# Kernel tuning notes

Measured on AMD Instinct MI355X. Metric: run time of the kernel, lower is better.

The kernel has to match this reference:

```python
import jax, jax.numpy as jnp
import numpy as np

BLANK = 4
NEG = -1.0e30  # log-space 'zero'


def _ctc_loss(log_probs, targets, input_lengths, target_lengths):
    # log_probs: (N, T, C) raw logits -> module applies log_softmax then transposes to (T, N, C)
    lp = jax.nn.log_softmax(log_probs, axis=-1)
    lp = jnp.transpose(lp, (1, 0, 2))  # (T, N, C)
    T, N, C = lp.shape
    S = targets.shape[1]
    L = 2 * S + 1  # extended label length (blanks interleaved)

    # extended label sequence: blank, y1, blank, y2, ..., yS, blank  -> (N, L)
    ext = jnp.full((N, L), BLANK, dtype=targets.dtype).at[:, 1::2].set(targets)

    # gather per-step log-probs of extended labels: (T, N, L)
    lp_ext = jnp.take_along_axis(lp, jnp.broadcast_to(ext[None], (T, N, L)), axis=2)

    # skip transition (k-2 -> k) allowed iff ext[k] != blank and ext[k] != ext[k-2]
    ext_m2 = jnp.pad(ext[:, :-2], ((0, 0), (2, 0)), constant_values=BLANK)
    skip = (ext != BLANK) & (ext != ext_m2)
    skip = skip.at[:, :2].set(False)

    # alpha at t=0: only positions 0 (blank) and 1 (first label) reachable
    alpha0 = jnp.full((N, L), NEG, dtype=lp.dtype)
    alpha0 = alpha0.at[:, 0].set(lp_ext[0, :, 0]).at[:, 1].set(lp_ext[0, :, 1])

    neg_col = jnp.full((N, 1), NEG, dtype=lp.dtype)

    def step(alpha, xs):
        t, lpe = xs  # lpe: (N, L)
        s1 = jnp.concatenate([neg_col, alpha[:, :-1]], axis=1)
        s2 = jnp.concatenate([neg_col, neg_col, alpha[:, :-2]], axis=1)
        a = jnp.logaddexp(alpha, s1)
        a = jnp.logaddexp(a, jnp.where(skip, s2, NEG))
        new = a + lpe
        # freeze alpha once past this sequence's input length
        alpha = jnp.where((t < input_lengths)[:, None], new, alpha)
        return alpha, None

    ts = jnp.arange(1, T)
    alpha, _ = jax.lax.scan(step, alpha0, (ts, lp_ext[1:]))

    idx = jnp.arange(N)
    last = 2 * target_lengths  # final blank position; last label is at 2L-1
    l_label = alpha[idx, last - 1]
    l_blank = alpha[idx, last]
    nll = -jnp.logaddexp(l_label, l_blank)  # per-sequence negative log-likelihood

    # reduction='mean': divide each loss by its target length, then mean over batch
    return jnp.mean(nll / target_lengths.astype(nll.dtype))


def setup_inputs() -> dict:
    key = jax.random.key(0)
    k1, k2, k3, k4 = jax.random.split(key, 4)
    N, T, C, S = 32, 1600, 1024, 200
    log_probs = jax.random.normal(k1, (N, T, C), dtype=jnp.float32)
    # targets in [0, C) excluding blank index 4
    t = jax.random.randint(k2, (N, S), 0, C - 1)
    targets = t + (t >= BLANK).astype(t.dtype)
    input_lengths = jax.random.randint(k3, (N,), 800, T + 1)
    target_lengths = jax.random.randint(k4, (N,), 50, S + 1)
    return {
        "log_probs": log_probs,
        "targets": targets,
        "input_lengths": input_lengths,
        "target_lengths": target_lengths,
    }


def reference(log_probs, targets, input_lengths, target_lengths):
    return _ctc_loss(log_probs, targets, input_lengths, target_lengths)
```

## Files before the change

kernel.cpp:

```cpp
#include <hip/hip_runtime.h>
#include <hip/hip_bf16.h>

#define N_    32
#define T_    1600
#define C_    1024
#define S_    200
#define L_    401
#define LP_   512
#define BLANK_ 4
#define LN2_  0.69314718055994531f
#define L2E_  1.44269504088896341f
#define DPF   8

#if __has_builtin(__builtin_amdgcn_exp2f)
#define EXP2(x) __builtin_amdgcn_exp2f(x)
#else
#define EXP2(x) exp2f(x)
#endif
#if __has_builtin(__builtin_amdgcn_rcpf)
#define RCP(x) __builtin_amdgcn_rcpf(x)
#else
#define RCP(x) (1.0f / (x))
#endif

__global__ __launch_bounds__(256)
void k_softmax_gather(const float* __restrict__ logits,
                      const int* __restrict__ targets,
                      const int* __restrict__ tgt_len,
                      float* __restrict__ P) {
  const int row  = blockIdx.x * 4 + (threadIdx.x >> 6);
  const int lane = threadIdx.x & 63;
  const int wv   = threadIdx.x >> 6;
  const int n    = row / T_;
  const float* x = logits + (size_t)row * C_;
  __shared__ float sh[4][C_];

  float4 v[4];
#pragma unroll
  for (int i = 0; i < 4; ++i)
    v[i] = reinterpret_cast<const float4*>(x)[i * 64 + lane];

  float mx = v[0].x;
#pragma unroll
  for (int i = 0; i < 4; ++i)
    mx = fmaxf(mx, fmaxf(fmaxf(v[i].x, v[i].y), fmaxf(v[i].z, v[i].w)));
#pragma unroll
  for (int i = 1; i < 64; i <<= 1) mx = fmaxf(mx, __shfl_xor(mx, i));

  float s = 0.0f;
#pragma unroll
  for (int i = 0; i < 4; ++i) {
    s += EXP2((v[i].x - mx) * L2E_) + EXP2((v[i].y - mx) * L2E_)
       + EXP2((v[i].z - mx) * L2E_) + EXP2((v[i].w - mx) * L2E_);
  }
#pragma unroll
  for (int i = 1; i < 64; i <<= 1) s += __shfl_xor(s, i);
  float rz = RCP(s);

#pragma unroll
  for (int i = 0; i < 4; ++i)
    reinterpret_cast<float4*>(sh[wv])[i * 64 + lane] = v[i];
  __syncthreads();

  const int* tg = targets + n * S_;
  const int lmax = 2 * tgt_len[n];
  float* out = P + (size_t)row * LP_;
#pragma unroll
  for (int i = 0; i < 8; ++i) {
    int l = lane + i * 64;
    float p = 0.0f;
    if (l <= lmax) {
      int c = (l & 1) ? tg[(l - 1) >> 1] : BLANK_;
      p = EXP2((sh[wv][c] - mx) * L2E_) * rz;
    }
    out[l] = p;
  }
}

__global__ __launch_bounds__(64)
void k_ctc(const float* __restrict__ P,
           const int* __restrict__ targets,
           const int* __restrict__ in_len,
           const int* __restrict__ tgt_len,
           float* __restrict__ nll_out) {
  const int n = blockIdx.x;
  const int lane = threadIdx.x;
  const int Tn = in_len[n];
  const float* g = P + (size_t)n * T_ * LP_;
  const int* tg = targets + n * S_;

  const int m0 = lane * 4;
  auto skv = [&](int m) -> double {
    int mi = (m >= 1 && m < S_) ? m : 1;
    return (m >= 1 && m < S_ && tg[mi] != tg[mi - 1]) ? 1.0 : 0.0;
  };
  const double sk1 = skv(m0), sk3 = skv(m0 + 1);
  const double sk5 = skv(m0 + 2), sk7 = skv(m0 + 3);

  double a0 = 0.0, a1 = 0.0, a2 = 0.0, a3 = 0.0;
  double a4 = 0.0, a5 = 0.0, a6 = 0.0, a7 = 0.0;
  double up = 0.0;
  if (lane == 0) { a0 = (double)g[0]; a1 = (double)g[1]; }
  int Etot = 0;

  const float* gl = g + lane * 8;
  float4 bA[DPF], bB[DPF];
#pragma unroll
  for (int d = 0; d < DPF; ++d) {
    int tt = 1 + d;
    bA[d] = *reinterpret_cast<const float4*>(gl + (size_t)tt * LP_);
    bB[d] = *reinterpret_cast<const float4*>(gl + (size_t)tt * LP_ + 4);
  }

  const int src = (lane + 63) & 63;

  auto step = [&](const float4& A, const float4& B) {
    double a7n = (a7 + a6 + sk7 * a5) * (double)B.w;
    double a6n = (a6 + a5) * (double)B.z;
    double upn = __shfl(a7n, src);
    double a5n = (a5 + a4 + sk5 * a3) * (double)B.y;
    double a4n = (a4 + a3) * (double)B.x;
    double a3n = (a3 + a2 + sk3 * a1) * (double)A.w;
    double a2n = (a2 + a1) * (double)A.z;
    double a1n = (a1 + a0 + sk1 * up) * (double)A.y;
    double a0n = (a0 + up) * (double)A.x;
    if (lane == 0) upn = 0.0;
    a0 = a0n; a1 = a1n; a2 = a2n; a3 = a3n;
    a4 = a4n; a5 = a5n; a6 = a6n; a7 = a7n;
    up = upn;
  };

  auto renorm = [&]() {
    int h = max(max(max(__double2hiint(a0), __double2hiint(a1)),
                    max(__double2hiint(a2), __double2hiint(a3))),
                max(max(__double2hiint(a4), __double2hiint(a5)),
                    max(__double2hiint(a6), __double2hiint(a7))));
#pragma unroll
    for (int i = 1; i < 64; i <<= 1) h = max(h, __shfl_xor(h, i));
    int R = 1021 - (h >> 20);
    a0 = ldexp(a0, R); a1 = ldexp(a1, R); a2 = ldexp(a2, R); a3 = ldexp(a3, R);
    a4 = ldexp(a4, R); a5 = ldexp(a5, R); a6 = ldexp(a6, R); a7 = ldexp(a7, R);
    up = ldexp(up, R);
    Etot -= R;
  };

  int t = 1;
  const int nsteps = Tn - 1;
  const int nfull = (nsteps / DPF) * DPF;
  int blk = 0;
  for (int s = 0; s < nfull; s += DPF) {
#pragma unroll
    for (int d = 0; d < DPF; ++d) {
      step(bA[d], bB[d]);
      int tt = t + DPF; if (tt > T_ - 1) tt = T_ - 1;
      bA[d] = *reinterpret_cast<const float4*>(gl + (size_t)tt * LP_);
      bB[d] = *reinterpret_cast<const float4*>(gl + (size_t)tt * LP_ + 4);
      ++t;
    }
    if ((++blk & 3) == 0) renorm();
  }
#pragma unroll
  for (int d = 0; d < DPF - 1; ++d) {
    if (t < Tn) { step(bA[d], bB[d]); ++t; }
  }

  __shared__ double sa[LP_];
  sa[lane * 8 + 0] = a0; sa[lane * 8 + 1] = a1;
  sa[lane * 8 + 2] = a2; sa[lane * 8 + 3] = a3;
  sa[lane * 8 + 4] = a4; sa[lane * 8 + 5] = a5;
  sa[lane * 8 + 6] = a6; sa[lane * 8 + 7] = a7;
  __syncthreads();
  if (lane == 0) {
    int tl = tgt_len[n];
    double v = sa[2 * tl - 1] + sa[2 * tl];
    int ee;
    double m = frexp(v, &ee);
    nll_out[n] = -LN2_ * ((float)(Etot + ee) + log2f((float)m));
  }
}

__global__ void k_final(const float* __restrict__ nll,
                        const int* __restrict__ tgt_len,
                        float* __restrict__ out) {
  int lane = threadIdx.x;
  float v = 0.0f;
  if (lane < N_) v = nll[lane] / (float)tgt_len[lane];
#pragma unroll
  for (int i = 1; i < 64; i <<= 1) v += __shfl_xor(v, i);
  if (lane == 0) out[0] = v * (1.0f / N_);
}

__global__ void k_sentinel(float* out) { out[0] = -12345.0f; }

extern "C" void kernel_launch(void* const* d_in, const int* in_sizes, int n_in,
                              void* d_out, int out_size, void* d_ws, size_t ws_size,
                              hipStream_t stream) {
  const float* logits = (const float*)d_in[0];
  const int* targets  = (const int*)d_in[1];
  const int* in_len   = (const int*)d_in[2];
  const int* tgt_len  = (const int*)d_in[3];
  float* out = (float*)d_out;

  size_t gbytes = (size_t)N_ * T_ * LP_ * sizeof(float);
  if (ws_size < gbytes + 256) {
    k_sentinel<<<1, 1, 0, stream>>>(out);
    return;
  }
  float* G = (float*)d_ws;
  float* nll = (float*)((char*)d_ws + gbytes);

  k_softmax_gather<<<(N_ * T_) / 4, 256, 0, stream>>>(logits, targets, tgt_len, G);
  k_ctc<<<N_, 64, 0, stream>>>(G, targets, in_len, tgt_len, nll);
  k_final<<<1, 64, 0, stream>>>(nll, tgt_len, out);
}
```

Baseline: 487.8 us.

## Stream CTC emission rows through an LDS ring via async global-to-LDS loads

Replaces the register-held 8-deep prefetch of per-timestep emission probabilities in the CTC recursion kernel with a 16-slot LDS ring. The ring is filled by global_load_lds direct copies issued 14 steps ahead, with explicit vmcnt waits, and the next step's row is read from LDS while the current step runs. The aim is to hide global memory latency on the serial alpha recursion without holding many float4 buffers in registers. In exchange it relies on hand-set waitcnt values and LDS slot reuse to stay correct, and it also sets launch bounds to one block per CU.

```diff
diff --git a/kernel.cpp b/kernel.cpp
--- a/kernel.cpp
+++ b/kernel.cpp
@@ -10,7 +10,8 @@
 #define BLANK_ 4
 #define LN2_  0.69314718055994531f
 #define L2E_  1.44269504088896341f
-#define DPF   8
+#define DEPTH 16
+#define PD    14
 
 #if __has_builtin(__builtin_amdgcn_exp2f)
 #define EXP2(x) __builtin_amdgcn_exp2f(x)
@@ -22,6 +23,12 @@
 #else
 #define RCP(x) (1.0f / (x))
 #endif
+
+__device__ __forceinline__ void gload_lds16(const float* gsrc, float* ldst) {
+  __builtin_amdgcn_global_load_lds(
+      (const __attribute__((address_space(1))) unsigned int*)gsrc,
+      (__attribute__((address_space(3))) unsigned int*)ldst, 16, 0, 0);
+}
 
 __global__ __launch_bounds__(256)
 void k_softmax_gather(const float* __restrict__ logits,
@@ -77,7 +84,7 @@
   }
 }
 
-__global__ __launch_bounds__(64)
+__global__ __launch_bounds__(64, 1)
 void k_ctc(const float* __restrict__ P,
            const int* __restrict__ targets,
            const int* __restrict__ in_len,
@@ -89,6 +96,9 @@
   const float* g = P + (size_t)n * T_ * LP_;
   const int* tg = targets + n * S_;
 
+  __shared__ __align__(16) float ring[DEPTH][LP_];
+  __shared__ double sa[LP_];
+
   const int m0 = lane * 4;
   auto skv = [&](int m) -> double {
     int mi = (m >= 1 && m < S_) ? m : 1;
@@ -102,15 +112,6 @@
   double up = 0.0;
   if (lane == 0) { a0 = (double)g[0]; a1 = (double)g[1]; }
   int Etot = 0;
-
-  const float* gl = g + lane * 8;
-  float4 bA[DPF], bB[DPF];
-#pragma unroll
-  for (int d = 0; d < DPF; ++d) {
-    int tt = 1 + d;
-    bA[d] = *reinterpret_cast<const float4*>(gl + (size_t)tt * LP_);
-    bB[d] = *reinterpret_cast<const float4*>(gl + (size_t)tt * LP_ + 4);
-  }
 
   const int src = (lane + 63) & 63;
 
@@ -144,27 +145,46 @@
     Etot -= R;
   };
 
+  auto stage = [&](int tt) {
+    int slot = tt & (DEPTH - 1);
+    if (tt > T_ - 1) tt = T_ - 1;
+    const float* s0 = g + (size_t)tt * LP_ + (lane << 3);
+    gload_lds16(s0,     &ring[slot][0]);
+    gload_lds16(s0 + 4, &ring[slot][256]);
+  };
+
+  auto dsread = [&](int tt, float4& A, float4& B) {
+    const float* b = &ring[tt & (DEPTH - 1)][lane << 2];
+    A = *reinterpret_cast<const float4*>(b);
+    B = *reinterpret_cast<const float4*>(b + 256);
+  };
+
+#pragma unroll
+  for (int r = 1; r <= PD; ++r) stage(r);
+  asm volatile("s_waitcnt vmcnt(26)" ::: "memory");
+  float4 A0, B0, A1, B1;
+  dsread(1, A0, B0);
+
+  const int nsteps = Tn - 1;
   int t = 1;
-  const int nsteps = Tn - 1;
-  const int nfull = (nsteps / DPF) * DPF;
-  int blk = 0;
-  for (int s = 0; s < nfull; s += DPF) {
-#pragma unroll
-    for (int d = 0; d < DPF; ++d) {
-      step(bA[d], bB[d]);
-      int tt = t + DPF; if (tt > T_ - 1) tt = T_ - 1;
-      bA[d] = *reinterpret_cast<const float4*>(gl + (size_t)tt * LP_);
-      bB[d] = *reinterpret_cast<const float4*>(gl + (size_t)tt * LP_ + 4);
-      ++t;
-    }
-    if ((++blk & 3) == 0) renorm();
-  }
-#pragma unroll
-  for (int d = 0; d < DPF - 1; ++d) {
-    if (t < Tn) { step(bA[d], bB[d]); ++t; }
-  }
-
-  __shared__ double sa[LP_];
+  while (t + 1 <= nsteps) {
+    stage(t + PD);
+    asm volatile("s_waitcnt vmcnt(26)" ::: "memory");
+    dsread(t + 1, A1, B1);
+    step(A0, B0);
+    if ((t & 31) == 0) renorm();
+    ++t;
+    stage(t + PD);
+    asm volatile("s_waitcnt vmcnt(26)" ::: "memory");
+    dsread(t + 1, A0, B0);
+    step(A1, B1);
+    if ((t & 31) == 0) renorm();
+    ++t;
+  }
+  if (t <= nsteps) {
+    step(A0, B0);
+  }
+
   sa[lane * 8 + 0] = a0; sa[lane * 8 + 1] = a1;
   sa[lane * 8 + 2] = a2; sa[lane * 8 + 3] = a3;
   sa[lane * 8 + 4] = a4; sa[lane * 8 + 5] = a5;
```

Measured after the change: 949.2 us. +94.6%, slower.
